# Kernel optimization log

Measured on AMD Instinct MI355X. Metric: run time of the kernel, lower is better.

## Reference

```python
import jax, jax.numpy as jnp
import numpy as np

B, T, D = 4, 8192, 512

def setup_inputs() -> dict:
    key = jax.random.key(0)
    k_x, k_w1, k_w2 = jax.random.split(key, 3)
    # Xavier-uniform-ish init for linear weights
    lim1 = np.sqrt(6.0 / (D + D)).astype(np.float32)
    lim2 = np.sqrt(6.0 / (D + 1)).astype(np.float32)
    return {
        "x": jax.random.normal(k_x, (B, T, D), dtype=jnp.float32),
        "W1": jax.random.uniform(k_w1, (D, D), dtype=jnp.float32, minval=-lim1, maxval=lim1),
        "b1": jnp.zeros((D,), dtype=jnp.float32),
        "w2": jax.random.uniform(k_w2, (D,), dtype=jnp.float32, minval=-lim2, maxval=lim2),
        "b2": jnp.zeros((), dtype=jnp.float32),
    }

def reference(x, W1, b1, w2, b2):
    h = jnp.tanh(jnp.einsum("btd,ed->bte", x, W1) + b1)   # [B,T,D]
    s = jnp.einsum("bte,e->bt", h, w2) + b2               # [B,T]
    # Causal prefix softmax-weighted sum:
    # context[b,t] = sum_{u<=t} softmax(s[b,:t+1])[u] * x[b,u]
    # Softmax is shift-invariant, so subtracting the global per-row max keeps
    # every prefix softmax exact while being numerically stable.
    m = jnp.max(s, axis=1, keepdims=True)                 # [B,1]
    e = jnp.exp(s - m)                                    # [B,T]
    den = jnp.cumsum(e, axis=1)                           # [B,T]
    num = jnp.cumsum(e[..., None] * x, axis=1)            # [B,T,D]
    context = num / den[..., None]                        # [B,T,D]
    return context
```

## Files before the change

kernel.cpp:

```cpp
#include <hip/hip_runtime.h>
#include <hip/hip_bf16.h>
#include <math.h>

#define BATCH 4
#define TLEN 8192
#define BT 32768
#define DIM 512
#define CHUNK 128
#define NCHUNK 64

#define BM 128
#define BN 128
#define BK 32

typedef _Float16 h8 __attribute__((ext_vector_type(8)));
typedef _Float16 h4 __attribute__((ext_vector_type(4)));
typedef float f4 __attribute__((ext_vector_type(4)));

__device__ __forceinline__ void gload_lds16(const _Float16* g, _Float16* l) {
    __builtin_amdgcn_global_load_lds(
        (const __attribute__((address_space(1))) void*)g,
        (__attribute__((address_space(3))) void*)l, 16, 0, 0);
}

__device__ __forceinline__ float fast_tanh(float z) {
    float u = __expf(2.0f * z);
    return 1.0f - __fdividef(2.0f, u + 1.0f);
}

__global__ __launch_bounds__(256) void convert_kernel(
    const float* __restrict__ x, const float* __restrict__ W1,
    _Float16* __restrict__ xh, _Float16* __restrict__ wh)
{
    const long i = (long)blockIdx.x * 256 + threadIdx.x;
    const long XD4 = (long)BT * DIM / 4;
    const long total4 = XD4 + (long)DIM * DIM / 4;
    if (i >= total4) return;
    float4 v;
    _Float16* dst;
    long j;
    if (i < XD4) { v = ((const float4*)x)[i];        dst = xh; j = i; }
    else         { v = ((const float4*)W1)[i - XD4]; dst = wh; j = i - XD4; }
    h4 o = { (_Float16)v.x, (_Float16)v.y, (_Float16)v.z, (_Float16)v.w };
    *(h4*)(dst + j * 4) = o;
}

__global__ __launch_bounds__(256, 4) void score_mfma_kernel(
    const _Float16* __restrict__ xh, const _Float16* __restrict__ wh,
    const float* __restrict__ b1, const float* __restrict__ w2,
    float* __restrict__ spart)
{
    __shared__ _Float16 Als[2][BM * BK];
    __shared__ _Float16 Bls[2][BM * BK];
    __shared__ float sred[2][BM];

    const int orig = blockIdx.x;
    const int wid  = (orig & 7) * 128 + (orig >> 3);
    const int bt = wid >> 2, be = wid & 3;
    const long trow0 = (long)bt * BM;
    const int  ecol0 = be * BN;

    const int tid  = threadIdx.x;
    const int lane = tid & 63;
    const int w    = tid >> 6;
    const int wr   = w >> 1;
    const int wc   = w & 1;
    const int l15  = lane & 15;
    const int lg   = lane >> 4;

    const int srow = w * 32 + (lane >> 2);
    const int skof = ((lane & 3) ^ (srow & 3)) * 8;
    const _Float16* ga = xh + (trow0 + srow) * DIM + skof;
    const _Float16* gb = wh + (long)(ecol0 + srow) * DIM + skof;
    _Float16* laA0 = &Als[0][w * 1024];
    _Float16* laB0 = &Bls[0][w * 1024];
    _Float16* laA1 = &Als[1][w * 1024];
    _Float16* laB1 = &Bls[1][w * 1024];

    const int koff = (lg ^ (l15 & 3)) * 8;

    float b1v[4], w2v[4];
    #pragma unroll
    for (int n = 0; n < 4; ++n) {
        int e = ecol0 + wc * 64 + n * 16 + l15;
        b1v[n] = b1[e];
        w2v[n] = w2[e];
    }
    asm volatile("s_waitcnt vmcnt(0)" ::: "memory");

    f4 acc[4][4];
    #pragma unroll
    for (int m = 0; m < 4; ++m)
        #pragma unroll
        for (int n = 0; n < 4; ++n) acc[m][n] = (f4){0.f, 0.f, 0.f, 0.f};

#define STAGE(A_, B_, k0_) {                         \
    gload_lds16(ga + (k0_),            (A_));        \
    gload_lds16(ga + 16 * DIM + (k0_), (A_) + 512);  \
    gload_lds16(gb + (k0_),            (B_));        \
    gload_lds16(gb + 16 * DIM + (k0_), (B_) + 512);  }

#define COMPUTE(bsel_) {                                                      \
    h8 afr[4], bfr[4];                                                        \
    _Pragma("unroll")                                                         \
    for (int m = 0; m < 4; ++m)                                               \
        afr[m] = *(const h8*)&Als[bsel_][(wr * 64 + m * 16 + l15) * BK + koff]; \
    _Pragma("unroll")                                                         \
    for (int n = 0; n < 4; ++n)                                               \
        bfr[n] = *(const h8*)&Bls[bsel_][(wc * 64 + n * 16 + l15) * BK + koff]; \
    _Pragma("unroll")                                                         \
    for (int m = 0; m < 4; ++m)                                               \
        _Pragma("unroll")                                                     \
        for (int n = 0; n < 4; ++n)                                           \
            acc[m][n] = __builtin_amdgcn_mfma_f32_16x16x32_f16(               \
                afr[m], bfr[n], acc[m][n], 0, 0, 0);                          }

    STAGE(laA0, laB0, 0);
    #pragma unroll 2
    for (int s = 0; s < 15; ++s) {
        if (s & 1) { STAGE(laA0, laB0, (s + 1) * BK); }
        else       { STAGE(laA1, laB1, (s + 1) * BK); }
        asm volatile("s_waitcnt vmcnt(4)" ::: "memory");
        __builtin_amdgcn_s_barrier();
        if (s & 1) { COMPUTE(1); } else { COMPUTE(0); }
        asm volatile("s_waitcnt lgkmcnt(0)" ::: "memory");
        __builtin_amdgcn_s_barrier();
    }
    asm volatile("s_waitcnt vmcnt(0)" ::: "memory");
    __builtin_amdgcn_s_barrier();
    COMPUTE(1);

    float pp[4][4];
    #pragma unroll
    for (int m = 0; m < 4; ++m)
        #pragma unroll
        for (int i = 0; i < 4; ++i) {
            float p = 0.f;
            #pragma unroll
            for (int n = 0; n < 4; ++n)
                p += w2v[n] * fast_tanh(acc[m][n][i] + b1v[n]);
            pp[m][i] = p;
        }
    #pragma unroll
    for (int off = 1; off < 16; off <<= 1)
        #pragma unroll
        for (int m = 0; m < 4; ++m)
            #pragma unroll
            for (int i = 0; i < 4; ++i)
                pp[m][i] += __shfl_xor(pp[m][i], off);
    __syncthreads();
    if (l15 == 0) {
        #pragma unroll
        for (int m = 0; m < 4; ++m)
            #pragma unroll
            for (int i = 0; i < 4; ++i)
                sred[wc][wr * 64 + m * 16 + lg * 4 + i] = pp[m][i];
    }
    __syncthreads();
    if (tid < BM)
        spart[(long)be * BT + trow0 + tid] = sred[0][tid] + sred[1][tid];
}

__global__ __launch_bounds__(128) void chunk_sum_kernel(
    const _Float16* __restrict__ xh, const float* __restrict__ spart,
    float* __restrict__ s_ws, float* __restrict__ csum,
    float* __restrict__ esum)
{
    __shared__ float el[CHUNK];
    __shared__ float wred[2];
    const int c = blockIdx.x, b = blockIdx.y;
    const int tid = threadIdx.x;
    const long bt = (long)b * TLEN + c * CHUNK + tid;

    float sv = spart[bt] + spart[BT + bt] + spart[2l * BT + bt] + spart[3l * BT + bt];
    s_ws[bt] = sv;
    float ev = __expf(sv);
    el[tid] = ev;
    float r = ev;
    #pragma unroll
    for (int off = 1; off < 64; off <<= 1) r += __shfl_xor(r, off);
    if ((tid & 63) == 0) wred[tid >> 6] = r;
    __syncthreads();
    if (tid == 0) esum[b * NCHUNK + c] = wred[0] + wred[1];

    const _Float16* xb = xh + ((long)b * TLEN + c * CHUNK) * DIM;
    float a0 = 0.f, a1 = 0.f, a2 = 0.f, a3 = 0.f;
    for (int t = 0; t < CHUNK; ++t) {
        h4 xv = *(const h4*)(xb + (long)t * DIM + tid * 4);
        float wgt = el[t];
        a0 += wgt * (float)xv[0];
        a1 += wgt * (float)xv[1];
        a2 += wgt * (float)xv[2];
        a3 += wgt * (float)xv[3];
    }
    float4 o = {a0, a1, a2, a3};
    ((float4*)(csum + ((long)(b * NCHUNK + c)) * DIM))[tid] = o;
}

__global__ __launch_bounds__(576) void chunk_scan_kernel(
    float* __restrict__ csum, float* __restrict__ esum)
{
    const int b = blockIdx.x;
    const int tid = threadIdx.x;
    if (tid < 512) {
        const int d = tid;
        float run = 0.f;
        #pragma unroll 8
        for (int c = 0; c < NCHUNK; ++c) {
            float* p = csum + ((long)(b * NCHUNK + c)) * DIM + d;
            float v = *p;
            *p = run;
            run += v;
        }
    } else {
        const int lane = tid - 512;
        float v = esum[b * NCHUNK + lane];
        const float own = v;
        #pragma unroll
        for (int off = 1; off < 64; off <<= 1) {
            float u = __shfl_up(v, off);
            if (lane >= off) v += u;
        }
        esum[b * NCHUNK + lane] = v - own;
    }
}

template <int FP16X>
__global__ __launch_bounds__(128) void context_kernel(
    const float* __restrict__ x, const _Float16* __restrict__ xh,
    const float* __restrict__ s_ws, const float* __restrict__ esum,
    const float* __restrict__ csum, float* __restrict__ out)
{
    __shared__ float el[CHUNK];
    const int c = blockIdx.x, b = blockIdx.y;
    const int tid = threadIdx.x;
    const long rowbase = (long)b * TLEN + c * CHUNK;
    el[tid] = __expf(s_ws[rowbase + tid]);
    __syncthreads();
    float dacc = esum[b * NCHUNK + c];
    float4* ob = (float4*)(out + rowbase * DIM);
    float4 acc = ((const float4*)(csum + ((long)(b * NCHUNK + c)) * DIM))[tid];
    for (int t = 0; t < CHUNK; ++t) {
        float xv0, xv1, xv2, xv3;
        if (FP16X) {
            h4 hv = *(const h4*)(xh + (rowbase + t) * DIM + tid * 4);
            xv0 = (float)hv[0]; xv1 = (float)hv[1];
            xv2 = (float)hv[2]; xv3 = (float)hv[3];
        } else {
            float4 fv = ((const float4*)(x + (rowbase + t) * DIM))[tid];
            xv0 = fv.x; xv1 = fv.y; xv2 = fv.z; xv3 = fv.w;
        }
        float wv = el[t];
        dacc += wv;
        acc.x += wv * xv0; acc.y += wv * xv1;
        acc.z += wv * xv2; acc.w += wv * xv3;
        float inv = __fdividef(1.0f, dacc);
        float4 o = {acc.x * inv, acc.y * inv, acc.z * inv, acc.w * inv};
        ob[t * (DIM / 4) + tid] = o;
    }
}

extern "C" void kernel_launch(void* const* d_in, const int* in_sizes, int n_in,
                              void* d_out, int out_size, void* d_ws, size_t ws_size,
                              hipStream_t stream)
{
    const float* x  = (const float*)d_in[0];
    const float* W1 = (const float*)d_in[1];
    const float* b1 = (const float*)d_in[2];
    const float* w2 = (const float*)d_in[3];
    float* out = (float*)d_out;

    float* ws   = (float*)d_ws;
    float* s_ws = ws;
    float* csum = ws + BT;
    float* esum = ws + BT + 4 * NCHUNK * DIM;
    const long ws_base_floats = BT + 4 * NCHUNK * DIM + 256;

    float* spart = out + 12l * 1024 * 1024;

    const size_t need = (size_t)ws_base_floats * 4
                      + ((size_t)BT * DIM + (size_t)DIM * DIM) * 2;
    const bool big_ws = ws_size >= need;

    _Float16* xh;
    _Float16* wh;
    if (big_ws) {
        xh = (_Float16*)(ws + ws_base_floats);
        wh = xh + (long)BT * DIM;
    } else {
        xh = (_Float16*)d_out;
        wh = xh + (long)BT * DIM;
    }

    const long total4 = ((long)BT * DIM + (long)DIM * DIM) / 4;
    const int convBlocks = (int)((total4 + 255) / 256);

    convert_kernel<<<convBlocks, 256, 0, stream>>>(x, W1, xh, wh);
    score_mfma_kernel<<<(BT / BM) * 4, 256, 0, stream>>>(xh, wh, b1, w2, spart);
    chunk_sum_kernel<<<dim3(NCHUNK, BATCH), 128, 0, stream>>>(xh, spart, s_ws, csum, esum);
    chunk_scan_kernel<<<BATCH, 576, 0, stream>>>(csum, esum);
    if (big_ws)
        context_kernel<1><<<dim3(NCHUNK, BATCH), 128, 0, stream>>>(x, xh, s_ws, esum, csum, out);
    else
        context_kernel<0><<<dim3(NCHUNK, BATCH), 128, 0, stream>>>(x, xh, s_ws, esum, csum, out);
}
```

Before: 79.52 us.

## Enlarge score GEMM tiles to 256x256 with 8 waves and MFMA-ordered LDS layout

Restructures the score GEMM from 128x128 tiles with BK=32 and 4 waves to 256x256 tiles with BK=64 and 8 waves, each wave computing 128x64. LDS is laid out in MFMA fragment order so A and B fragments load contiguously per lane, and compute is wrapped in s_setprio. The number of E-column partials drops from 4 to 2, so chunk_sum reads fewer partial sums. This raises arithmetic intensity and reduces redundant x reads, at the cost of more LDS (128KB), more accumulator registers, and only 256 blocks, which lowers occupancy and parallelism.

```diff
diff --git a/kernel.cpp b/kernel.cpp
--- a/kernel.cpp
+++ b/kernel.cpp
@@ -8,10 +8,6 @@
 #define DIM 512
 #define CHUNK 128
 #define NCHUNK 64
-
-#define BM 128
-#define BN 128
-#define BK 32
 
 typedef _Float16 h8 __attribute__((ext_vector_type(8)));
 typedef _Float16 h4 __attribute__((ext_vector_type(4)));
@@ -45,94 +41,102 @@
     *(h4*)(dst + j * 4) = o;
 }
 
-__global__ __launch_bounds__(256, 4) void score_mfma_kernel(
+__global__ __launch_bounds__(512, 2) void score_mfma_kernel(
     const _Float16* __restrict__ xh, const _Float16* __restrict__ wh,
     const float* __restrict__ b1, const float* __restrict__ w2,
     float* __restrict__ spart)
 {
-    __shared__ _Float16 Als[2][BM * BK];
-    __shared__ _Float16 Bls[2][BM * BK];
-    __shared__ float sred[2][BM];
+    __shared__ _Float16 Als[2 * 16384];
+    __shared__ _Float16 Bls[2 * 16384];
+    float* sred = (float*)Als;
 
     const int orig = blockIdx.x;
-    const int wid  = (orig & 7) * 128 + (orig >> 3);
-    const int bt = wid >> 2, be = wid & 3;
-    const long trow0 = (long)bt * BM;
-    const int  ecol0 = be * BN;
+    const int wid  = (orig & 7) * 32 + (orig >> 3);
+    const int bt = wid >> 1, be = wid & 1;
+    const long trow0 = (long)bt * 256;
+    const int  ecol0 = be * 256;
 
     const int tid  = threadIdx.x;
     const int lane = tid & 63;
     const int w    = tid >> 6;
-    const int wr   = w >> 1;
-    const int wc   = w & 1;
+    const int wm   = w >> 2;
+    const int wn   = w & 3;
     const int l15  = lane & 15;
-    const int lg   = lane >> 4;
-
-    const int srow = w * 32 + (lane >> 2);
-    const int skof = ((lane & 3) ^ (srow & 3)) * 8;
-    const _Float16* ga = xh + (trow0 + srow) * DIM + skof;
-    const _Float16* gb = wh + (long)(ecol0 + srow) * DIM + skof;
-    _Float16* laA0 = &Als[0][w * 1024];
-    _Float16* laB0 = &Bls[0][w * 1024];
-    _Float16* laA1 = &Als[1][w * 1024];
-    _Float16* laB1 = &Bls[1][w * 1024];
-
-    const int koff = (lg ^ (l15 & 3)) * 8;
 
     float b1v[4], w2v[4];
     #pragma unroll
     for (int n = 0; n < 4; ++n) {
-        int e = ecol0 + wc * 64 + n * 16 + l15;
+        int e = ecol0 + wn * 64 + n * 16 + l15;
         b1v[n] = b1[e];
         w2v[n] = w2[e];
     }
-    asm volatile("s_waitcnt vmcnt(0)" ::: "memory");
-
-    f4 acc[4][4];
-    #pragma unroll
-    for (int m = 0; m < 4; ++m)
+
+    f4 acc[8][4];
+    #pragma unroll
+    for (int m = 0; m < 8; ++m)
         #pragma unroll
         for (int n = 0; n < 4; ++n) acc[m][n] = (f4){0.f, 0.f, 0.f, 0.f};
 
-#define STAGE(A_, B_, k0_) {                         \
-    gload_lds16(ga + (k0_),            (A_));        \
-    gload_lds16(ga + 16 * DIM + (k0_), (A_) + 512);  \
-    gload_lds16(gb + (k0_),            (B_));        \
-    gload_lds16(gb + 16 * DIM + (k0_), (B_) + 512);  }
-
-#define COMPUTE(bsel_) {                                                      \
-    h8 afr[4], bfr[4];                                                        \
+#define STAGE_TILE(buf_, kt_) {                                               \
+    _Float16* A_ = Als + (buf_) * 16384;                                      \
+    _Float16* B_ = Bls + (buf_) * 16384;                                      \
     _Pragma("unroll")                                                         \
-    for (int m = 0; m < 4; ++m)                                               \
-        afr[m] = *(const h8*)&Als[bsel_][(wr * 64 + m * 16 + l15) * BK + koff]; \
+    for (int jj = 0; jj < 4; ++jj) {                                          \
+        const int c_  = jj * 512 + tid;                                       \
+        const int row = ((c_ >> 7) << 4) + (c_ & 15);                         \
+        const int kg  = (c_ >> 4) & 7;                                        \
+        gload_lds16(xh + (trow0 + row) * DIM + (kt_) * 64 + kg * 8,           \
+                    A_ + c_ * 8);                                             \
+        gload_lds16(wh + (long)(ecol0 + row) * DIM + (kt_) * 64 + kg * 8,     \
+                    B_ + c_ * 8);                                             \
+    }                                                                         }
+
+#define COMPUTE_TILE(buf_) {                                                  \
+    const _Float16* A_ = Als + (buf_) * 16384;                                \
+    const _Float16* B_ = Bls + (buf_) * 16384;                                \
     _Pragma("unroll")                                                         \
-    for (int n = 0; n < 4; ++n)                                               \
-        bfr[n] = *(const h8*)&Bls[bsel_][(wc * 64 + n * 16 + l15) * BK + koff]; \
-    _Pragma("unroll")                                                         \
-    for (int m = 0; m < 4; ++m)                                               \
+    for (int kh = 0; kh < 2; ++kh) {                                          \
+        h8 bfr[4];                                                            \
         _Pragma("unroll")                                                     \
         for (int n = 0; n < 4; ++n)                                           \
-            acc[m][n] = __builtin_amdgcn_mfma_f32_16x16x32_f16(               \
-                afr[m], bfr[n], acc[m][n], 0, 0, 0);                          }
-
-    STAGE(laA0, laB0, 0);
-    #pragma unroll 2
-    for (int s = 0; s < 15; ++s) {
-        if (s & 1) { STAGE(laA0, laB0, (s + 1) * BK); }
-        else       { STAGE(laA1, laB1, (s + 1) * BK); }
-        asm volatile("s_waitcnt vmcnt(4)" ::: "memory");
-        __builtin_amdgcn_s_barrier();
-        if (s & 1) { COMPUTE(1); } else { COMPUTE(0); }
+            bfr[n] = *(const h8*)&B_[((wn * 4 + n) * 128 + kh * 64 + lane) * 8]; \
+        _Pragma("unroll")                                                     \
+        for (int mh = 0; mh < 2; ++mh) {                                      \
+            h8 afr[4];                                                        \
+            _Pragma("unroll")                                                 \
+            for (int mm = 0; mm < 4; ++mm)                                    \
+                afr[mm] = *(const h8*)&A_[((wm * 8 + mh * 4 + mm) * 128       \
+                                           + kh * 64 + lane) * 8];            \
+            _Pragma("unroll")                                                 \
+            for (int mm = 0; mm < 4; ++mm)                                    \
+                _Pragma("unroll")                                             \
+                for (int n = 0; n < 4; ++n)                                   \
+                    acc[mh * 4 + mm][n] =                                     \
+                        __builtin_amdgcn_mfma_f32_16x16x32_f16(               \
+                            afr[mm], bfr[n], acc[mh * 4 + mm][n], 0, 0, 0);   \
+        }                                                                     \
+    }                                                                         }
+
+    STAGE_TILE(0, 0);
+    asm volatile("s_waitcnt vmcnt(0)" ::: "memory");
+    __builtin_amdgcn_s_barrier();
+
+    #pragma unroll
+    for (int t = 0; t < 8; ++t) {
+        const int cb = t & 1;
+        if (t < 7) STAGE_TILE(cb ^ 1, t + 1);
+        __builtin_amdgcn_s_setprio(1);
+        COMPUTE_TILE(cb);
+        __builtin_amdgcn_s_setprio(0);
         asm volatile("s_waitcnt lgkmcnt(0)" ::: "memory");
         __builtin_amdgcn_s_barrier();
-    }
-    asm volatile("s_waitcnt vmcnt(0)" ::: "memory");
-    __builtin_amdgcn_s_barrier();
-    COMPUTE(1);
-
-    float pp[4][4];
-    #pragma unroll
-    for (int m = 0; m < 4; ++m)
+        if (t < 7) asm volatile("s_waitcnt vmcnt(0)" ::: "memory");
+        __builtin_amdgcn_s_barrier();
+    }
+
+    float pp[8][4];
+    #pragma unroll
+    for (int m = 0; m < 8; ++m)
         #pragma unroll
         for (int i = 0; i < 4; ++i) {
             float p = 0.f;
@@ -144,21 +148,23 @@
     #pragma unroll
     for (int off = 1; off < 16; off <<= 1)
         #pragma unroll
-        for (int m = 0; m < 4; ++m)
+        for (int m = 0; m < 8; ++m)
             #pragma unroll
             for (int i = 0; i < 4; ++i)
                 pp[m][i] += __shfl_xor(pp[m][i], off);
-    __syncthreads();
     if (l15 == 0) {
-        #pragma unroll
-        for (int m = 0; m < 4; ++m)
+        const int lg = lane >> 4;
+        #pragma unroll
+        for (int m = 0; m < 8; ++m)
             #pragma unroll
             for (int i = 0; i < 4; ++i)
-                sred[wc][wr * 64 + m * 16 + lg * 4 + i] = pp[m][i];
+                sred[wn * 256 + wm * 128 + m * 16 + lg * 4 + i] = pp[m][i];
     }
     __syncthreads();
-    if (tid < BM)
-        spart[(long)be * BT + trow0 + tid] = sred[0][tid] + sred[1][tid];
+    if (tid < 256) {
+        float v = sred[tid] + sred[256 + tid] + sred[512 + tid] + sred[768 + tid];
+        spart[(long)be * BT + trow0 + tid] = v;
+    }
 }
 
 __global__ __launch_bounds__(128) void chunk_sum_kernel(
@@ -172,7 +178,7 @@
     const int tid = threadIdx.x;
     const long bt = (long)b * TLEN + c * CHUNK + tid;
 
-    float sv = spart[bt] + spart[BT + bt] + spart[2l * BT + bt] + spart[3l * BT + bt];
+    float sv = spart[bt] + spart[BT + bt];
     s_ws[bt] = sv;
     float ev = __expf(sv);
     el[tid] = ev;
@@ -296,7 +302,7 @@
     const int convBlocks = (int)((total4 + 255) / 256);
 
     convert_kernel<<<convBlocks, 256, 0, stream>>>(x, W1, xh, wh);
-    score_mfma_kernel<<<(BT / BM) * 4, 256, 0, stream>>>(xh, wh, b1, w2, spart);
+    score_mfma_kernel<<<(BT / 256) * 2, 512, 0, stream>>>(xh, wh, b1, w2, spart);
     chunk_sum_kernel<<<dim3(NCHUNK, BATCH), 128, 0, stream>>>(xh, spart, s_ws, csum, esum);
     chunk_scan_kernel<<<BATCH, 576, 0, stream>>>(csum, esum);
     if (big_ws)
```

Result: slower. 83.58 us (+5.1%).
